# Performance work log

Measured on AMD Instinct MI355X. Metric: run time of the kernel, lower is better.

## Reference

```python
import jax, jax.numpy as jnp
import numpy as np

N_EMBD = 1024
N_HEADS = 16
HEAD_DIM = N_EMBD // N_HEADS
T = 1024
B = 1
WINDOW = 64
LM_STRIDE = 64


def _build_neigh_idx(T, window, stride, n_heads, seed):
    """Per-head neighbor index [H, T, D], padded with -1.

    Neighbors of i: cycle prev/next (sorted), causal window i-window..i-1,
    landmarks j%stride==0 with j<i, then self; deduped preserving order.
    Matches _build_neighbors_index with a single random cycle per head.
    """
    rng = np.random.default_rng(seed)
    n_land = (T + stride - 1) // stride
    D = 2 + window + n_land + 1  # max_cycle_deg + window + landmarks + self
    out = np.full((n_heads, T, D), -1, dtype=np.int64)
    lands = list(range(0, T, stride))
    for h in range(n_heads):
        perm = rng.permutation(T)
        inv = np.argsort(perm)
        prev = perm[(inv - 1) % T]
        nxt = perm[(inv + 1) % T]
        for i in range(T):
            neigh = sorted({int(prev[i]), int(nxt[i])})
            neigh += list(range(max(0, i - window), i))
            neigh += [j for j in lands if j < i]
            neigh.append(i)
            seen = set()
            ded = []
            for j in neigh:
                if j not in seen:
                    ded.append(j)
                    seen.add(j)
            out[h, i, :len(ded)] = ded
    return out


def setup_inputs() -> dict:
    key = jax.random.key(0)
    k1, k2, k3 = jax.random.split(key, 3)
    scale = 1.0 / np.sqrt(N_EMBD)
    x = jax.random.normal(k1, (B, T, N_EMBD), dtype=jnp.float32)
    Wqkv = jax.random.normal(k2, (N_EMBD, 3 * N_EMBD), dtype=jnp.float32) * scale
    Wout = jax.random.normal(k3, (N_EMBD, N_EMBD), dtype=jnp.float32) * scale
    neigh_idx = jnp.asarray(_build_neigh_idx(T, WINDOW, LM_STRIDE, N_HEADS, seed=0))
    return {"x": x, "Wqkv": Wqkv, "Wout": Wout, "neigh_idx": neigh_idx}


def reference(x, Wqkv, Wout, neigh_idx):
    Bv, Tv, C = x.shape
    H, dh = N_HEADS, HEAD_DIM
    qkv = x @ Wqkv  # [B,T,3C]
    q, k, v = jnp.split(qkv, 3, axis=-1)
    q = q.reshape(Bv, Tv, H, dh).transpose(0, 2, 1, 3)  # [B,H,T,dh]
    k = k.reshape(Bv, Tv, H, dh).transpose(0, 2, 1, 3)
    v = v.reshape(Bv, Tv, H, dh).transpose(0, 2, 1, 3)

    safe = jnp.clip(neigh_idx, 0)  # [H,T,D]
    h_ix = jnp.arange(H)[:, None, None]
    k_g = k[:, h_ix, safe, :]  # [B,H,T,D,dh]
    v_g = v[:, h_ix, safe, :]

    scores = jnp.einsum("bhtd,bhtnd->bhtn", q, k_g) / np.sqrt(dh)
    valid = neigh_idx >= 0
    causal = safe <= jnp.arange(Tv)[None, :, None]
    mask = valid & causal  # [H,T,D]; self always present -> rows non-empty
    scores = jnp.where(mask[None], scores, -jnp.inf)
    w = jax.nn.softmax(scores, axis=-1)  # [B,H,T,D]
    y = jnp.einsum("bhtn,bhtnd->bhtd", w, v_g)  # [B,H,T,dh]
    y = y.transpose(0, 2, 1, 3).reshape(Bv, Tv, C)
    return y @ Wout
```

## Files before the change

kernel.cpp:

```cpp
#include <hip/hip_runtime.h>
#include <math.h>

#define NH 16
#define TT 1024
#define HD 64
#define NE 1024

typedef unsigned int u32;
typedef unsigned short u16;
typedef __bf16 bf16x8 __attribute__((ext_vector_type(8)));
typedef float f32x4 __attribute__((ext_vector_type(4)));

__device__ inline u16 f2bf(float f) {
  u32 u = __builtin_bit_cast(u32, f);
  u32 r = (u + 0x7fffu + ((u >> 16) & 1u)) >> 16;
  return (u16)r;
}
__device__ inline float bf2f(u16 h) {
  return __builtin_bit_cast(float, (u32)h << 16);
}
__device__ inline void gload16(const void* g, void* l) {
  __builtin_amdgcn_global_load_lds((const __attribute__((address_space(1))) void*)g,
                                   (__attribute__((address_space(3))) void*)l, 16, 0, 0);
}

__global__ __launch_bounds__(256) void prep(const float* __restrict__ x,
                                            const float* __restrict__ Wqkv,
                                            const float* __restrict__ Wout,
                                            u16* __restrict__ xb,
                                            u16* __restrict__ WqkvT,
                                            u16* __restrict__ WoutT) {
  __shared__ float tile[64][65];
  const int tid = threadIdx.x;
  const int bx = blockIdx.x;
  if (bx < 1024) {
    int i = bx * 256 + tid;
    float4 f = ((const float4*)x)[i];
    ushort4 o = {f2bf(f.x), f2bf(f.y), f2bf(f.z), f2bf(f.w)};
    ((ushort4*)xb)[i] = o;
    return;
  }
  int b = bx - 1024;
  int nb = b & 63, kb = b >> 6;
  const float* W; u16* WT; int N, n0;
  if (nb < 48) { W = Wqkv; WT = WqkvT; N = 3 * NE; n0 = nb * 64; }
  else         { W = Wout; WT = WoutT; N = NE;     n0 = (nb - 48) * 64; }
  const int k0 = kb * 64;
#pragma unroll
  for (int it = 0; it < 16; ++it) {
    int idx = it * 256 + tid;
    int r = idx >> 6, c = idx & 63;
    tile[r][c] = W[(size_t)(k0 + r) * N + n0 + c];
  }
  __syncthreads();
#pragma unroll
  for (int it = 0; it < 16; ++it) {
    int idx = it * 256 + tid;
    int nn = idx >> 6, kk = idx & 63;
    WT[(size_t)(n0 + nn) * NE + k0 + kk] = f2bf(tile[kk][nn]);
  }
}

template<int R>
__device__ __forceinline__ void stage_rows(const u16* __restrict__ G, int ldk,
                                           u16* L, int tid) {
#pragma unroll
  for (int it = 0; it < R / 32; ++it) {
    int idx = it * 256 + tid;
    int r = idx >> 3, kg = idx & 7;
    gload16(G + (size_t)r * ldk + ((kg ^ (r & 7)) << 3), L + (idx << 3));
  }
}

template<int SPLITK, int NT>
__global__ __launch_bounds__(256) void gemm_bt(const u16* __restrict__ A,
                                               const u16* __restrict__ Bt,
                                               float* __restrict__ C,
                                               int M, int N, int K) {
  __shared__ u16 As[2][128 * 64];
  __shared__ u16 Bs[2][NT * 64];
  const int tid = threadIdx.x;
  const int lane = tid & 63;
  const int wv = tid >> 6;
  const int wm = wv >> 1, wn = wv & 1;
  const int row0 = blockIdx.y * 128;
  const int col0 = blockIdx.x * NT;
  const int sk = blockIdx.z;
  const int Klen = K / SPLITK;
  const int nsteps = Klen >> 6;
  constexpr int NI = NT / 32;

  const u16* Ab = A + (size_t)row0 * K + sk * Klen;
  const u16* Bb = Bt + (size_t)col0 * K + sk * Klen;

  f32x4 acc[4][NI] = {};

  stage_rows<128>(Ab, K, As[0], tid);
  stage_rows<NT>(Bb, K, Bs[0], tid);
  __syncthreads();

  int buf = 0;
  for (int ks = 0; ks < nsteps; ++ks) {
    if (ks + 1 < nsteps) {
      stage_rows<128>(Ab + (ks + 1) * 64, K, As[buf ^ 1], tid);
      stage_rows<NT>(Bb + (ks + 1) * 64, K, Bs[buf ^ 1], tid);
    }
#pragma unroll
    for (int half = 0; half < 2; ++half) {
      const int kk = half * 32;
      bf16x8 af[4], bfr[NI];
#pragma unroll
      for (int mi = 0; mi < 4; ++mi) {
        int r = wm * 64 + mi * 16 + (lane & 15);
        int c = (kk >> 3) + (lane >> 4);
        af[mi] = *(const bf16x8*)&As[buf][(r * 8 + (c ^ (r & 7))) * 8];
      }
#pragma unroll
      for (int ni = 0; ni < NI; ++ni) {
        int r = wn * (NT / 2) + ni * 16 + (lane & 15);
        int c = (kk >> 3) + (lane >> 4);
        bfr[ni] = *(const bf16x8*)&Bs[buf][(r * 8 + (c ^ (r & 7))) * 8];
      }
#pragma unroll
      for (int mi = 0; mi < 4; ++mi)
#pragma unroll
        for (int ni = 0; ni < NI; ++ni)
          acc[mi][ni] = __builtin_amdgcn_mfma_f32_16x16x32_bf16(af[mi], bfr[ni], acc[mi][ni], 0, 0, 0);
    }
    __syncthreads();
    buf ^= 1;
  }

  const int rbase = row0 + wm * 64 + (lane >> 4) * 4;
  const int cbase = col0 + wn * (NT / 2) + (lane & 15);
  float* Cp = C + (size_t)sk * M * N;
#pragma unroll
  for (int mi = 0; mi < 4; ++mi)
#pragma unroll
    for (int ni = 0; ni < NI; ++ni)
#pragma unroll
      for (int r = 0; r < 4; ++r)
        Cp[(size_t)(rbase + mi * 16 + r) * N + cbase + ni * 16] = acc[mi][ni][r];
}

__global__ __launch_bounds__(256) void reduce_qkv(const float* __restrict__ Pg,
                                                  u16* __restrict__ qkvb) {
  const int t = blockIdx.y;
  const int n4 = blockIdx.x * 256 + threadIdx.x;
  const int i = t * 768 + n4;
  f32x4 a = ((const f32x4*)Pg)[i];
  a += ((const f32x4*)(Pg + (size_t)TT * 3 * NE))[i];
  int n = n4 * 4;
  int which = n >> 10, h = (n & 1023) >> 6, d = n & 63;
  ushort4 o = {f2bf(a[0]), f2bf(a[1]), f2bf(a[2]), f2bf(a[3])};
  *(ushort4*)&qkvb[(size_t)which * (NH * TT * HD) + (size_t)h * (TT * HD) +
                   (size_t)t * HD + d] = o;
}

__global__ __launch_bounds__(256) void reduce_out(const float* __restrict__ P,
                                                  float* __restrict__ out) {
  int i = blockIdx.x * 256 + threadIdx.x;
  f32x4 a = ((const f32x4*)P)[i];
  a += ((const f32x4*)(P + (size_t)TT * NE))[i];
  a += ((const f32x4*)(P + 2 * (size_t)TT * NE))[i];
  a += ((const f32x4*)(P + 3 * (size_t)TT * NE))[i];
  ((f32x4*)out)[i] = a;
}

__global__ __launch_bounds__(256) void attn4(const u16* __restrict__ qkv,
                                             const int* __restrict__ nidx,
                                             u16* __restrict__ y, int D) {
  __shared__ __align__(16) u16 Qs[16 * 64];
  __shared__ __align__(16) u16 Ks[128 * 64];
  __shared__ __align__(16) u16 Vt[64 * 128];
  __shared__ int pn_l[32];
  __shared__ int colj[128];
  __shared__ float rinv[16];
  float* S = (float*)Ks;
  u16* P = (u16*)((char*)Ks + 8448);

  const int tid = threadIdx.x;
  const int lane = tid & 63;
  const int wv = tid >> 6;
  const int h = blockIdx.y;
  const int t0 = blockIdx.x * 16;

  const u16* qh = qkv + (size_t)h * TT * HD;
  const u16* kh = qkv + (size_t)NH * TT * HD + (size_t)h * TT * HD;
  const u16* vh = qkv + 2 * (size_t)NH * TT * HD + (size_t)h * TT * HD;

  if (tid < 32) pn_l[tid] = nidx[((size_t)h * TT + t0 + (tid >> 1)) * D + (tid & 1)];
  __syncthreads();

  if (tid < 128) {
    int c = tid, j;
    if (c < 80) {
      j = t0 - 64 + c;
      if (j < 0) j = -1;
    } else if (c < 96) {
      j = (c - 80) * 64;
      if (j >= t0 - 64) j = -1;
    } else {
      int s = c - 96;
      j = pn_l[s];
      bool keep = (j < t0 - 64) && ((j & 63) != 0);
      if (keep)
        for (int s2 = 0; s2 < s; ++s2)
          if (pn_l[s2] == j) { keep = false; break; }
      if (!keep) j = -1;
    }
    colj[c] = j;
  }
  __syncthreads();

  if (tid < 128) {
    int row = tid >> 3, slot = tid & 7, ch = slot ^ (row & 7);
    gload16(qh + (size_t)(t0 + row) * HD + ch * 8, Qs + tid * 8);
  }
  uint4 vreg[4];
#pragma unroll
  for (int it = 0; it < 4; ++it) {
    int idx = it * 256 + tid;
    int col = idx >> 3, slot = idx & 7, ch = slot ^ (col & 7);
    int j = colj[col]; if (j < 0) j = 0;
    gload16(kh + (size_t)j * HD + ch * 8, Ks + idx * 8);
  }
#pragma unroll
  for (int it = 0; it < 4; ++it) {
    int idx = it * 256 + tid;
    int col = idx >> 3, ch = idx & 7;
    int j = colj[col]; if (j < 0) j = 0;
    vreg[it] = *(const uint4*)(vh + (size_t)j * HD + ch * 8);
  }
  __syncthreads();

  f32x4 sc[2] = {};
  bf16x8 af[2];
#pragma unroll
  for (int half = 0; half < 2; ++half) {
    int row = lane & 15;
    int chunk = 4 * half + (lane >> 4);
    af[half] = *(const bf16x8*)&Qs[(row * 8 + (chunk ^ (row & 7))) * 8];
  }
#pragma unroll
  for (int p = 0; p < 2; ++p) {
    int col = 16 * (2 * wv + p) + (lane & 15);
#pragma unroll
    for (int half = 0; half < 2; ++half) {
      int chunk = 4 * half + (lane >> 4);
      bf16x8 bfv = *(const bf16x8*)&Ks[(col * 8 + (chunk ^ (col & 7))) * 8];
      sc[p] = __builtin_amdgcn_mfma_f32_16x16x32_bf16(af[half], bfv, sc[p], 0, 0, 0);
    }
  }
  __syncthreads();

#pragma unroll
  for (int p = 0; p < 2; ++p) {
    int col = 16 * (2 * wv + p) + (lane & 15);
    int j = colj[col];
#pragma unroll
    for (int r = 0; r < 4; ++r) {
      int row = (lane >> 4) * 4 + r;
      int i = t0 + row;
      int p0 = pn_l[2 * row], p1 = pn_l[2 * row + 1];
      bool m;
      if (col < 80)      m = (j >= 0) && (j <= i) &&
                             ((i - j) <= 64 || (j & 63) == 0 || j == p0 || j == p1);
      else if (col < 96) m = (j >= 0);
      else               m = (j >= 0) && (j == p0 || j == p1);
      S[row * 132 + col] = m ? ((float)sc[p][r]) * 0.125f : -1e30f;
    }
  }
  __syncthreads();

  {
    int row = tid >> 4, q = tid & 15;
    float v[8];
    float mx = -3e38f;
#pragma unroll
    for (int e = 0; e < 8; ++e) {
      v[e] = S[row * 132 + 8 * q + e];
      mx = fmaxf(mx, v[e]);
    }
#pragma unroll
    for (int off = 1; off < 16; off <<= 1) mx = fmaxf(mx, __shfl_xor(mx, off, 64));
    float sum = 0.f;
#pragma unroll
    for (int e = 0; e < 8; ++e) {
      v[e] = __expf(v[e] - mx);
      sum += v[e];
    }
#pragma unroll
    for (int off = 1; off < 16; off <<= 1) sum += __shfl_xor(sum, off, 64);
    if (q == 0) rinv[row] = 1.0f / sum;
    u32 w0 = (u32)f2bf(v[0]) | ((u32)f2bf(v[1]) << 16);
    u32 w1 = (u32)f2bf(v[2]) | ((u32)f2bf(v[3]) << 16);
    u32 w2 = (u32)f2bf(v[4]) | ((u32)f2bf(v[5]) << 16);
    u32 w3 = (u32)f2bf(v[6]) | ((u32)f2bf(v[7]) << 16);
    uint4 pk = {w0, w1, w2, w3};
    *(uint4*)&P[row * 128 + ((q ^ (row & 7)) << 3)] = pk;
  }

#pragma unroll
  for (int it = 0; it < 4; ++it) {
    int idx = it * 256 + tid;
    int col = idx >> 3, ch = idx & 7;
    const u32* vw = (const u32*)&vreg[it];
#pragma unroll
    for (int e = 0; e < 8; ++e) {
      int d = ch * 8 + e;
      u16 val = (e & 1) ? (u16)(vw[e >> 1] >> 16) : (u16)(vw[e >> 1] & 0xffffu);
      int swz = (col >> 3) ^ e ^ ch;
      Vt[d * 128 + swz * 8 + (col & 7)] = val;
    }
  }
  __syncthreads();

  f32x4 oacc = {};
#pragma unroll
  for (int ks2 = 0; ks2 < 4; ++ks2) {
    int rowp = lane & 15;
    int chp = ks2 * 4 + (lane >> 4);
    bf16x8 pa = *(const bf16x8*)&P[rowp * 128 + ((chp ^ (rowp & 7)) << 3)];
    int dd = wv * 16 + (lane & 15);
    int swz = chp ^ (dd & 7) ^ ((dd >> 3) & 7);
    bf16x8 vb = *(const bf16x8*)&Vt[dd * 128 + swz * 8];
    oacc = __builtin_amdgcn_mfma_f32_16x16x32_bf16(pa, vb, oacc, 0, 0, 0);
  }
  {
    int dd = wv * 16 + (lane & 15);
#pragma unroll
    for (int r = 0; r < 4; ++r) {
      int row = (lane >> 4) * 4 + r;
      y[(size_t)(t0 + row) * NE + h * HD + dd] = f2bf(oacc[r] * rinv[row]);
    }
  }
}

extern "C" void kernel_launch(void* const* d_in, const int* in_sizes, int n_in,
                              void* d_out, int out_size, void* d_ws, size_t ws_size,
                              hipStream_t stream) {
  const float* x    = (const float*)d_in[0];
  const float* Wqkv = (const float*)d_in[1];
  const float* Wout = (const float*)d_in[2];
  const int*   nidx = (const int*)d_in[3];
  float* out = (float*)d_out;

  u16* ws16  = (u16*)d_ws;
  u16* xb    = ws16;
  u16* WqkvT = ws16 + 1048576;
  u16* WoutT = ws16 + 4194304;
  u16* qkvb  = ws16 + 5242880;
  float* Pg   = (float*)((char*)d_ws + (16u << 20));
  float* Pout = (float*)((char*)d_ws + (40u << 20));

  const int D = in_sizes[3] / (NH * TT);

  prep<<<2048, 256, 0, stream>>>(x, Wqkv, Wout, xb, WqkvT, WoutT);

  gemm_bt<2, 64><<<dim3(48, 8, 2), 256, 0, stream>>>(xb, WqkvT, Pg, TT, 3 * NE, NE);
  reduce_qkv<<<dim3(3, TT), 256, 0, stream>>>(Pg, qkvb);

  attn4<<<dim3(TT / 16, NH), 256, 0, stream>>>(qkvb, nidx, xb, D);

  gemm_bt<4, 64><<<dim3(16, 8, 4), 256, 0, stream>>>(xb, WoutT, Pout, TT, NE, NE);
  reduce_out<<<TT * NE / 4 / 256, 256, 0, stream>>>(Pout, out);
}
```

Before: 53.80 us.

## Replace split-K GEMMs and reduce kernels with direct-write GEMMs

Both GEMMs drop split-K and shrink the M tile from 128 to 64 rows, so the grid keeps enough blocks without partial sums. The QKV GEMM now converts to bf16 and scatters into the head-major q/k/v layout in its epilogue, and the output GEMM writes fp32 straight to the result. This removes the two reduction kernels, their launches and the fp32 partial-buffer traffic. In exchange each block runs the full K loop, and the epilogue stores are scalar and strided.

Result: faster. 46.46 us (-13.6%).

```diff
diff --git a/kernel.cpp b/kernel.cpp
--- a/kernel.cpp
+++ b/kernel.cpp
@@ -72,46 +72,44 @@
   }
 }
 
-template<int SPLITK, int NT>
-__global__ __launch_bounds__(256) void gemm_bt(const u16* __restrict__ A,
-                                               const u16* __restrict__ Bt,
-                                               float* __restrict__ C,
-                                               int M, int N, int K) {
-  __shared__ u16 As[2][128 * 64];
+template<int MODE, int NT>
+__global__ __launch_bounds__(256) void gemm_direct(const u16* __restrict__ A,
+                                                   const u16* __restrict__ Bt,
+                                                   void* __restrict__ Cv,
+                                                   int M, int N, int K) {
+  __shared__ u16 As[2][64 * 64];
   __shared__ u16 Bs[2][NT * 64];
   const int tid = threadIdx.x;
   const int lane = tid & 63;
   const int wv = tid >> 6;
   const int wm = wv >> 1, wn = wv & 1;
-  const int row0 = blockIdx.y * 128;
+  const int row0 = blockIdx.y * 64;
   const int col0 = blockIdx.x * NT;
-  const int sk = blockIdx.z;
-  const int Klen = K / SPLITK;
-  const int nsteps = Klen >> 6;
+  const int nsteps = K >> 6;
   constexpr int NI = NT / 32;
 
-  const u16* Ab = A + (size_t)row0 * K + sk * Klen;
-  const u16* Bb = Bt + (size_t)col0 * K + sk * Klen;
-
-  f32x4 acc[4][NI] = {};
-
-  stage_rows<128>(Ab, K, As[0], tid);
+  const u16* Ab = A + (size_t)row0 * K;
+  const u16* Bb = Bt + (size_t)col0 * K;
+
+  f32x4 acc[2][NI] = {};
+
+  stage_rows<64>(Ab, K, As[0], tid);
   stage_rows<NT>(Bb, K, Bs[0], tid);
   __syncthreads();
 
   int buf = 0;
   for (int ks = 0; ks < nsteps; ++ks) {
     if (ks + 1 < nsteps) {
-      stage_rows<128>(Ab + (ks + 1) * 64, K, As[buf ^ 1], tid);
+      stage_rows<64>(Ab + (ks + 1) * 64, K, As[buf ^ 1], tid);
       stage_rows<NT>(Bb + (ks + 1) * 64, K, Bs[buf ^ 1], tid);
     }
 #pragma unroll
     for (int half = 0; half < 2; ++half) {
       const int kk = half * 32;
-      bf16x8 af[4], bfr[NI];
-#pragma unroll
-      for (int mi = 0; mi < 4; ++mi) {
-        int r = wm * 64 + mi * 16 + (lane & 15);
+      bf16x8 af[2], bfr[NI];
+#pragma unroll
+      for (int mi = 0; mi < 2; ++mi) {
+        int r = wm * 32 + mi * 16 + (lane & 15);
         int c = (kk >> 3) + (lane >> 4);
         af[mi] = *(const bf16x8*)&As[buf][(r * 8 + (c ^ (r & 7))) * 8];
       }
@@ -122,7 +120,7 @@
         bfr[ni] = *(const bf16x8*)&Bs[buf][(r * 8 + (c ^ (r & 7))) * 8];
       }
 #pragma unroll
-      for (int mi = 0; mi < 4; ++mi)
+      for (int mi = 0; mi < 2; ++mi)
 #pragma unroll
         for (int ni = 0; ni < NI; ++ni)
           acc[mi][ni] = __builtin_amdgcn_mfma_f32_16x16x32_bf16(af[mi], bfr[ni], acc[mi][ni], 0, 0, 0);
@@ -131,40 +129,27 @@
     buf ^= 1;
   }
 
-  const int rbase = row0 + wm * 64 + (lane >> 4) * 4;
+  const int rbase = row0 + wm * 32 + (lane >> 4) * 4;
   const int cbase = col0 + wn * (NT / 2) + (lane & 15);
-  float* Cp = C + (size_t)sk * M * N;
-#pragma unroll
-  for (int mi = 0; mi < 4; ++mi)
-#pragma unroll
-    for (int ni = 0; ni < NI; ++ni)
-#pragma unroll
-      for (int r = 0; r < 4; ++r)
-        Cp[(size_t)(rbase + mi * 16 + r) * N + cbase + ni * 16] = acc[mi][ni][r];
-}
-
-__global__ __launch_bounds__(256) void reduce_qkv(const float* __restrict__ Pg,
-                                                  u16* __restrict__ qkvb) {
-  const int t = blockIdx.y;
-  const int n4 = blockIdx.x * 256 + threadIdx.x;
-  const int i = t * 768 + n4;
-  f32x4 a = ((const f32x4*)Pg)[i];
-  a += ((const f32x4*)(Pg + (size_t)TT * 3 * NE))[i];
-  int n = n4 * 4;
-  int which = n >> 10, h = (n & 1023) >> 6, d = n & 63;
-  ushort4 o = {f2bf(a[0]), f2bf(a[1]), f2bf(a[2]), f2bf(a[3])};
-  *(ushort4*)&qkvb[(size_t)which * (NH * TT * HD) + (size_t)h * (TT * HD) +
-                   (size_t)t * HD + d] = o;
-}
-
-__global__ __launch_bounds__(256) void reduce_out(const float* __restrict__ P,
-                                                  float* __restrict__ out) {
-  int i = blockIdx.x * 256 + threadIdx.x;
-  f32x4 a = ((const f32x4*)P)[i];
-  a += ((const f32x4*)(P + (size_t)TT * NE))[i];
-  a += ((const f32x4*)(P + 2 * (size_t)TT * NE))[i];
-  a += ((const f32x4*)(P + 3 * (size_t)TT * NE))[i];
-  ((f32x4*)out)[i] = a;
+#pragma unroll
+  for (int mi = 0; mi < 2; ++mi) {
+#pragma unroll
+    for (int ni = 0; ni < NI; ++ni) {
+      int n = cbase + ni * 16;
+#pragma unroll
+      for (int r = 0; r < 4; ++r) {
+        int t = rbase + mi * 16 + r;
+        float val = acc[mi][ni][r];
+        if (MODE == 0) {
+          ((float*)Cv)[(size_t)t * N + n] = val;
+        } else {
+          int which = n >> 10, h = (n & 1023) >> 6, d = n & 63;
+          ((u16*)Cv)[(size_t)which * (NH * TT * HD) + (size_t)h * (TT * HD) +
+                     (size_t)t * HD + d] = f2bf(val);
+        }
+      }
+    }
+  }
 }
 
 __global__ __launch_bounds__(256) void attn4(const u16* __restrict__ qkv,
@@ -351,18 +336,14 @@
   u16* WqkvT = ws16 + 1048576;
   u16* WoutT = ws16 + 4194304;
   u16* qkvb  = ws16 + 5242880;
-  float* Pg   = (float*)((char*)d_ws + (16u << 20));
-  float* Pout = (float*)((char*)d_ws + (40u << 20));
 
   const int D = in_sizes[3] / (NH * TT);
 
   prep<<<2048, 256, 0, stream>>>(x, Wqkv, Wout, xb, WqkvT, WoutT);
 
-  gemm_bt<2, 64><<<dim3(48, 8, 2), 256, 0, stream>>>(xb, WqkvT, Pg, TT, 3 * NE, NE);
-  reduce_qkv<<<dim3(3, TT), 256, 0, stream>>>(Pg, qkvb);
+  gemm_direct<1, 64><<<dim3(48, 16), 256, 0, stream>>>(xb, WqkvT, qkvb, TT, 3 * NE, NE);
 
   attn4<<<dim3(TT / 16, NH), 256, 0, stream>>>(qkvb, nidx, xb, D);
 
-  gemm_bt<4, 64><<<dim3(16, 8, 4), 256, 0, stream>>>(xb, WoutT, Pout, TT, NE, NE);
-  reduce_out<<<TT * NE / 4 / 256, 256, 0, stream>>>(Pout, out);
-}
+  gemm_direct<0, 32><<<dim3(32, 16), 256, 0, stream>>>(xb, WoutT, out, TT, NE, NE);
+}
```

## Fuse split-K QKV reduction into attention gather and widen GEMM tiles

Applied to the files above, without the earlier changes.

Removes the reduce_qkv kernel. The attention kernel now reads the two fp32 split-K partials directly for Q, K and V, sums them and converts to bf16 while staging into LDS. The V transpose is reorganised so each thread holds four consecutive columns and writes packed uint2 values into the transposed tile. Both GEMMs switch to 128-wide N tiles with half the grid width. This saves one launch and a bf16 intermediate round-trip, but each gathered row is now loaded as fp32 twice, so the attention kernel moves about four times the bytes per gathered row.

Measured after the change: 61.06 us. 13.5% more time.

```diff
diff --git a/kernel.cpp b/kernel.cpp
--- a/kernel.cpp
+++ b/kernel.cpp
@@ -16,12 +16,19 @@
   u32 r = (u + 0x7fffu + ((u >> 16) & 1u)) >> 16;
   return (u16)r;
 }
+__device__ inline u32 pk2bf(float lo, float hi) {
+  return (u32)f2bf(lo) | ((u32)f2bf(hi) << 16);
+}
 __device__ inline float bf2f(u16 h) {
   return __builtin_bit_cast(float, (u32)h << 16);
 }
 __device__ inline void gload16(const void* g, void* l) {
   __builtin_amdgcn_global_load_lds((const __attribute__((address_space(1))) void*)g,
                                    (__attribute__((address_space(3))) void*)l, 16, 0, 0);
+}
+__device__ inline u16 h16(uint4 v, int e) {
+  u32 w = ((const u32*)&v)[e >> 1];
+  return (e & 1) ? (u16)(w >> 16) : (u16)(w & 0xffffu);
 }
 
 __global__ __launch_bounds__(256) void prep(const float* __restrict__ x,
@@ -143,20 +150,6 @@
         Cp[(size_t)(rbase + mi * 16 + r) * N + cbase + ni * 16] = acc[mi][ni][r];
 }
 
-__global__ __launch_bounds__(256) void reduce_qkv(const float* __restrict__ Pg,
-                                                  u16* __restrict__ qkvb) {
-  const int t = blockIdx.y;
-  const int n4 = blockIdx.x * 256 + threadIdx.x;
-  const int i = t * 768 + n4;
-  f32x4 a = ((const f32x4*)Pg)[i];
-  a += ((const f32x4*)(Pg + (size_t)TT * 3 * NE))[i];
-  int n = n4 * 4;
-  int which = n >> 10, h = (n & 1023) >> 6, d = n & 63;
-  ushort4 o = {f2bf(a[0]), f2bf(a[1]), f2bf(a[2]), f2bf(a[3])};
-  *(ushort4*)&qkvb[(size_t)which * (NH * TT * HD) + (size_t)h * (TT * HD) +
-                   (size_t)t * HD + d] = o;
-}
-
 __global__ __launch_bounds__(256) void reduce_out(const float* __restrict__ P,
                                                   float* __restrict__ out) {
   int i = blockIdx.x * 256 + threadIdx.x;
@@ -167,7 +160,7 @@
   ((f32x4*)out)[i] = a;
 }
 
-__global__ __launch_bounds__(256) void attn4(const u16* __restrict__ qkv,
+__global__ __launch_bounds__(256) void attn6(const float* __restrict__ Pg,
                                              const int* __restrict__ nidx,
                                              u16* __restrict__ y, int D) {
   __shared__ __align__(16) u16 Qs[16 * 64];
@@ -185,11 +178,23 @@
   const int h = blockIdx.y;
   const int t0 = blockIdx.x * 16;
 
-  const u16* qh = qkv + (size_t)h * TT * HD;
-  const u16* kh = qkv + (size_t)NH * TT * HD + (size_t)h * TT * HD;
-  const u16* vh = qkv + 2 * (size_t)NH * TT * HD + (size_t)h * TT * HD;
+  const float* Pg2 = Pg + (size_t)TT * 3 * NE;
+  const int qoff = h * HD;
+  const int koff = NE + h * HD;
+  const int voff = 2 * NE + h * HD;
 
   if (tid < 32) pn_l[tid] = nidx[((size_t)h * TT + t0 + (tid >> 1)) * D + (tid & 1)];
+
+  if (tid < 128) {
+    int row = tid >> 3, slot = tid & 7, ch = slot ^ (row & 7);
+    const float* s1 = Pg  + (size_t)(t0 + row) * (3 * NE) + qoff + ch * 8;
+    const float* s2 = Pg2 + (size_t)(t0 + row) * (3 * NE) + qoff + ch * 8;
+    float4 a0 = *(const float4*)s1, a1 = *(const float4*)(s1 + 4);
+    float4 b0 = *(const float4*)s2, b1 = *(const float4*)(s2 + 4);
+    uint4 pk = {pk2bf(a0.x + b0.x, a0.y + b0.y), pk2bf(a0.z + b0.z, a0.w + b0.w),
+                pk2bf(a1.x + b1.x, a1.y + b1.y), pk2bf(a1.z + b1.z, a1.w + b1.w)};
+    *(uint4*)&Qs[tid * 8] = pk;
+  }
   __syncthreads();
 
   if (tid < 128) {
@@ -213,24 +218,34 @@
   }
   __syncthreads();
 
-  if (tid < 128) {
-    int row = tid >> 3, slot = tid & 7, ch = slot ^ (row & 7);
-    gload16(qh + (size_t)(t0 + row) * HD + ch * 8, Qs + tid * 8);
-  }
-  uint4 vreg[4];
 #pragma unroll
   for (int it = 0; it < 4; ++it) {
     int idx = it * 256 + tid;
     int col = idx >> 3, slot = idx & 7, ch = slot ^ (col & 7);
     int j = colj[col]; if (j < 0) j = 0;
-    gload16(kh + (size_t)j * HD + ch * 8, Ks + idx * 8);
-  }
+    const float* s1 = Pg  + (size_t)j * (3 * NE) + koff + ch * 8;
+    const float* s2 = Pg2 + (size_t)j * (3 * NE) + koff + ch * 8;
+    float4 a0 = *(const float4*)s1, a1 = *(const float4*)(s1 + 4);
+    float4 b0 = *(const float4*)s2, b1 = *(const float4*)(s2 + 4);
+    uint4 pk = {pk2bf(a0.x + b0.x, a0.y + b0.y), pk2bf(a0.z + b0.z, a0.w + b0.w),
+                pk2bf(a1.x + b1.x, a1.y + b1.y), pk2bf(a1.z + b1.z, a1.w + b1.w)};
+    *(uint4*)&Ks[idx * 8] = pk;
+  }
+  const int d0 = (tid & 7) * 8;
+  const int cq = tid >> 3;
+  uint4 vreg[4];
 #pragma unroll
   for (int it = 0; it < 4; ++it) {
-    int idx = it * 256 + tid;
-    int col = idx >> 3, ch = idx & 7;
+    int col = cq * 4 + it;
     int j = colj[col]; if (j < 0) j = 0;
-    vreg[it] = *(const uint4*)(vh + (size_t)j * HD + ch * 8);
+    const float* s1 = Pg  + (size_t)j * (3 * NE) + voff + d0;
+    const float* s2 = Pg2 + (size_t)j * (3 * NE) + voff + d0;
+    float4 a0 = *(const float4*)s1, a1 = *(const float4*)(s1 + 4);
+    float4 b0 = *(const float4*)s2, b1 = *(const float4*)(s2 + 4);
+    vreg[it].x = pk2bf(a0.x + b0.x, a0.y + b0.y);
+    vreg[it].y = pk2bf(a0.z + b0.z, a0.w + b0.w);
+    vreg[it].z = pk2bf(a1.x + b1.x, a1.y + b1.y);
+    vreg[it].w = pk2bf(a1.z + b1.z, a1.w + b1.w);
   }
   __syncthreads();
 
@@ -293,26 +308,19 @@
 #pragma unroll
     for (int off = 1; off < 16; off <<= 1) sum += __shfl_xor(sum, off, 64);
     if (q == 0) rinv[row] = 1.0f / sum;
-    u32 w0 = (u32)f2bf(v[0]) | ((u32)f2bf(v[1]) << 16);
-    u32 w1 = (u32)f2bf(v[2]) | ((u32)f2bf(v[3]) << 16);
-    u32 w2 = (u32)f2bf(v[4]) | ((u32)f2bf(v[5]) << 16);
-    u32 w3 = (u32)f2bf(v[6]) | ((u32)f2bf(v[7]) << 16);
-    uint4 pk = {w0, w1, w2, w3};
+    uint4 pk = {pk2bf(v[0], v[1]), pk2bf(v[2], v[3]),
+                pk2bf(v[4], v[5]), pk2bf(v[6], v[7])};
     *(uint4*)&P[row * 128 + ((q ^ (row & 7)) << 3)] = pk;
   }
 
 #pragma unroll
-  for (int it = 0; it < 4; ++it) {
-    int idx = it * 256 + tid;
-    int col = idx >> 3, ch = idx & 7;
-    const u32* vw = (const u32*)&vreg[it];
-#pragma unroll
-    for (int e = 0; e < 8; ++e) {
-      int d = ch * 8 + e;
-      u16 val = (e & 1) ? (u16)(vw[e >> 1] >> 16) : (u16)(vw[e >> 1] & 0xffffu);
-      int swz = (col >> 3) ^ e ^ ch;
-      Vt[d * 128 + swz * 8 + (col & 7)] = val;
-    }
+  for (int e = 0; e < 8; ++e) {
+    int d = d0 + e;
+    u32 lo = (u32)h16(vreg[0], e) | ((u32)h16(vreg[1], e) << 16);
+    u32 hi = (u32)h16(vreg[2], e) | ((u32)h16(vreg[3], e) << 16);
+    int oswz = (cq >> 1) ^ (d & 7) ^ ((d >> 3) & 7);
+    uint2 pk2 = {lo, hi};
+    *(uint2*)&Vt[d * 128 + oswz * 8 + (cq & 1) * 4] = pk2;
   }
   __syncthreads();
 
@@ -350,7 +358,6 @@
   u16* xb    = ws16;
   u16* WqkvT = ws16 + 1048576;
   u16* WoutT = ws16 + 4194304;
-  u16* qkvb  = ws16 + 5242880;
   float* Pg   = (float*)((char*)d_ws + (16u << 20));
   float* Pout = (float*)((char*)d_ws + (40u << 20));
 
@@ -358,11 +365,10 @@
 
   prep<<<2048, 256, 0, stream>>>(x, Wqkv, Wout, xb, WqkvT, WoutT);
 
-  gemm_bt<2, 64><<<dim3(48, 8, 2), 256, 0, stream>>>(xb, WqkvT, Pg, TT, 3 * NE, NE);
-  reduce_qkv<<<dim3(3, TT), 256, 0, stream>>>(Pg, qkvb);
-
-  attn4<<<dim3(TT / 16, NH), 256, 0, stream>>>(qkvb, nidx, xb, D);
-
-  gemm_bt<4, 64><<<dim3(16, 8, 4), 256, 0, stream>>>(xb, WoutT, Pout, TT, NE, NE);
+  gemm_bt<2, 128><<<dim3(24, 8, 2), 256, 0, stream>>>(xb, WqkvT, Pg, TT, 3 * NE, NE);
+
+  attn6<<<dim3(TT / 16, NH), 256, 0, stream>>>(Pg, nidx, xb, D);
+
+  gemm_bt<4, 128><<<dim3(8, 8, 4), 256, 0, stream>>>(xb, WoutT, Pout, TT, NE, NE);
   reduce_out<<<TT * NE / 4 / 256, 256, 0, stream>>>(Pout, out);
 }
```
